# Kernel tuning notes

Measured on AMD Instinct MI355X. Metric: run time of the kernel, lower is better.

## Reference

```python
import jax, jax.numpy as jnp
import numpy as np

B, S, H = 8, 2048, 1024
NEG = -1e10


def setup_inputs() -> dict:
    key = jax.random.key(0)
    ks = jax.random.split(key, 8)
    scale = 1.0 / np.sqrt(H)
    return {
        "x": jax.random.normal(ks[0], (B, S, H), dtype=jnp.float32),
        "pad_mask": jax.random.randint(ks[1], (B, S), 0, 2, dtype=jnp.int32),
        "Wq": jax.random.uniform(ks[2], (H, H), jnp.float32, -scale, scale),
        "bq": jax.random.uniform(ks[3], (H,), jnp.float32, -scale, scale),
        "Wk": jax.random.uniform(ks[4], (H, H), jnp.float32, -scale, scale),
        "bk": jax.random.uniform(ks[5], (H,), jnp.float32, -scale, scale),
        "Wv": jax.random.uniform(ks[6], (H, H), jnp.float32, -scale, scale),
        "bv": jax.random.uniform(ks[7], (H,), jnp.float32, -scale, scale),
    }


def reference(x, pad_mask, Wq, bq, Wk, bk, Wv, bv):
    # Linear projections (torch Linear: x @ W.T + b)
    q = x @ Wq.T + bq  # [B,S,H]
    k = x @ Wk.T + bk
    v = x @ Wv.T + bv
    weight = jnp.einsum("bid,bjd->bij", q, k)  # [B,S,S]
    seq = x.shape[1]
    # causal mask (strictly upper triangular) + padding mask over key positions
    causal = jnp.triu(jnp.ones((seq, seq), dtype=jnp.float32), k=1)  # [S,S]
    pad = pad_mask.astype(jnp.float32)[:, None, :]  # [B,1,S] -> key axis
    mask = (causal[None, :, :] + pad) > 0  # [B,S,S]
    # torch code fills BEFORE scaling; replicate exactly
    weight = jnp.where(mask, NEG, weight)
    score = jax.nn.softmax(weight / jnp.sqrt(jnp.float32(weight.shape[-1] * 0 + x.shape[-1])), axis=-1)
    return jnp.einsum("bij,bjd->bid", score, v)
```

## Files before the change

### kernel.cpp

```cpp
#include <hip/hip_runtime.h>

typedef __attribute__((ext_vector_type(8))) short short8;
typedef __attribute__((ext_vector_type(4))) short short4v;
typedef __attribute__((ext_vector_type(4))) float float4v;

typedef const __attribute__((address_space(1))) unsigned int* gptr_t;
typedef __attribute__((address_space(3))) unsigned int* lptr_t;

__device__ __forceinline__ unsigned short f2bf(float f) {
  unsigned u = __float_as_uint(f);
  u += 0x7FFFu + ((u >> 16) & 1u);
  return (unsigned short)(u >> 16);
}
__device__ __forceinline__ float bf2f(unsigned short h) {
  return __uint_as_float(((unsigned)h) << 16);
}

__global__ __launch_bounds__(256) void cvt_bf16_kernel(const float* __restrict__ in,
                                                       unsigned short* __restrict__ out,
                                                       int n4) {
  int i = blockIdx.x * 256 + threadIdx.x;
  if (i >= n4) return;
  float4v v = ((const float4v*)in)[i];
  short4v o;
  o[0] = (short)f2bf(v[0]);
  o[1] = (short)f2bf(v[1]);
  o[2] = (short)f2bf(v[2]);
  o[3] = (short)f2bf(v[3]);
  ((short4v*)out)[i] = o;
}

__global__ __launch_bounds__(256) void compact_kernel(const int* __restrict__ pad,
                                                      int* __restrict__ jmap,
                                                      int* __restrict__ cntb,
                                                      float* __restrict__ mean_x) {
  int b = blockIdx.x;
  const int* prow = pad + b * 2048;
  int t = threadIdx.x;
  float4v z = {0.f, 0.f, 0.f, 0.f};
  ((float4v*)(mean_x + b * 1024))[t] = z;
  int base = t * 8;
  int ind[8], incl[8];
  int s = 0;
#pragma unroll
  for (int e = 0; e < 8; ++e) {
    ind[e] = (prow[base + e] == 0);
    s += ind[e];
    incl[e] = s;
  }
  int lane = t & 63, wv = t >> 6;
  int v = s;
#pragma unroll
  for (int off = 1; off < 64; off <<= 1) {
    int u = __shfl_up(v, off);
    if (lane >= off) v += u;
  }
  __shared__ int wsum[4];
  if (lane == 63) wsum[wv] = v;
  __syncthreads();
  int wbase = 0;
  for (int w = 0; w < wv; ++w) wbase += wsum[w];
  int excl_base = wbase + v - s;
#pragma unroll
  for (int e = 0; e < 8; ++e) {
    int cnt_i = excl_base + incl[e];
    cntb[b * 2048 + base + e] = cnt_i;
    if (ind[e]) jmap[b * 2048 + cnt_i - 1] = base + e;
  }
}

__global__ __launch_bounds__(256) void gatherX_kernel(const unsigned short* __restrict__ xb,
                                                      const int* __restrict__ jmap,
                                                      const int* __restrict__ cntb,
                                                      unsigned short* __restrict__ xc) {
  int jc = blockIdx.x, b = blockIdx.y;
  int Nc = cntb[b * 2048 + 2047];
  int W = (Nc + 127) & ~127;
  if (jc >= W) return;
  short4v* dst = (short4v*)(xc + ((size_t)(b * 2048 + jc)) * 1024);
  if (jc < Nc) {
    int j = jmap[b * 2048 + jc];
    const short4v* src = (const short4v*)(xb + ((size_t)(b * 2048 + j)) * 1024);
    dst[threadIdx.x] = src[threadIdx.x];
  } else {
    short4v z = {0, 0, 0, 0};
    dst[threadIdx.x] = z;
  }
}

__global__ __launch_bounds__(256) void meanx_kernel(const unsigned short* __restrict__ xb,
                                                    float* __restrict__ mean_x) {
  int b = blockIdx.x, hblk = blockIdx.y, iblk = blockIdx.z;
  int h = hblk * 256 + threadIdx.x;
  float s = 0.f;
  const unsigned short* base = xb + ((size_t)b * 2048 + (size_t)iblk * 256) * 1024 + h;
  for (int i = 0; i < 256; ++i) s += bf2f(base[(size_t)i * 1024]);
  atomicAdd(&mean_x[b * 1024 + h], s);
}

__global__ __launch_bounds__(256) void gemv_kernel(const float* __restrict__ mean_x,
                                                   const unsigned short* __restrict__ wv,
                                                   const float* __restrict__ bv,
                                                   float* __restrict__ fixmean) {
  int b = blockIdx.x, dblk = blockIdx.y;
  int d = dblk * 256 + threadIdx.x;
  const unsigned short* wrow = wv + (size_t)d * 1024;
  const float* mx = mean_x + b * 1024;
  float s = 0.f;
  for (int h = 0; h < 1024; h += 8) {
    short8 w = *(const short8*)(wrow + h);
#pragma unroll
    for (int e = 0; e < 8; ++e) s += mx[h + e] * bf2f(((const unsigned short*)&w)[e]);
  }
  fixmean[b * 1024 + d] = s * (1.0f / 2048.0f) + bv[d];
}

template <int MODE>
__global__ __launch_bounds__(256, 4) void gemm_bt_kernel(
    const unsigned short* __restrict__ A, const unsigned short* __restrict__ B,
    const float* __restrict__ bias1, const float* __restrict__ bias2,
    void* __restrict__ C, unsigned short* __restrict__ C2, const int* __restrict__ cnt,
    int K, int lda, int ldb, int ldc, size_t sA, size_t sB, size_t sC) {
  int bx = blockIdx.x, by = blockIdx.y, bz = blockIdx.z;
  if (MODE == 0) {
    int wg = by * 8 + bx;
    int s = (wg & 7) * 128 + (wg >> 3);
    bx = s & 7;
    by = s >> 3;
  }
  if (MODE == 1) {
    int wg = by * 16 + bx;
    int s = (wg & 7) * 32 + (wg >> 3);
    bx = s & 15;
    by = s >> 4;
  }
  int Kend = K;
  if (MODE == 1) {
    int Nc = cnt[(bz << 11) + 2047];
    if (by * 128 >= Nc) return;
  }
  if (MODE == 2) {
    int tc = cnt[(bz << 11) + (by * 128 + 127)];
    if (bx * 128 >= tc) return;
  }
  if (MODE == 3) {
    int tc = cnt[(bz << 11) + (by * 128 + 127)];
    Kend = (tc + 63) & ~63;
  }

  __shared__ __align__(16) char lds[32768];
  char* ldsA = lds;
  char* ldsB = lds + 16384;

  int tid = threadIdx.x;
  int wave = tid >> 6, lane = tid & 63;
  int lm = lane & 15, g = lane >> 4;
  int wm = wave >> 1, wn = wave & 1;
  int swl = (lm & 7) << 4;

  float4v acc[4][4];
#pragma unroll
  for (int i = 0; i < 4; ++i)
#pragma unroll
    for (int j = 0; j < 4; ++j) {
      float4v z = {0.f, 0.f, 0.f, 0.f};
      acc[i][j] = z;
    }

  const char* Abase = (const char*)(A + sA * (size_t)bz + (size_t)(by * 128) * (size_t)lda);
  const char* Bbase = (const char*)(B + sB * (size_t)bz + (size_t)(bx * 128) * (size_t)ldb);
  size_t strideA = (size_t)lda * 2u;
  size_t strideB = (size_t)ldb * 2u;

  int Lbase = wave * 1024 + lane * 16;

  for (int kt = 0; kt < Kend; kt += 64) {
#pragma unroll
    for (int c = 0; c < 4; ++c) {
      int L = c * 4096 + Lbase;
      int row = L >> 7;
      int lb = (L & 127) ^ ((row & 7) << 4);
      const char* ga = Abase + (size_t)row * strideA + (size_t)(kt * 2) + lb;
      __builtin_amdgcn_global_load_lds((gptr_t)(const void*)ga,
                                       (lptr_t)(void*)(ldsA + c * 4096 + wave * 1024), 16, 0, 0);
      const char* gb = Bbase + (size_t)row * strideB + (size_t)(kt * 2) + lb;
      __builtin_amdgcn_global_load_lds((gptr_t)(const void*)gb,
                                       (lptr_t)(void*)(ldsB + c * 4096 + wave * 1024), 16, 0, 0);
    }
    __syncthreads();

#pragma unroll
    for (int k0 = 0; k0 < 64; k0 += 32) {
      short8 af[4], bfv[4];
      int b0 = (k0 * 2 + 16 * g) ^ swl;
#pragma unroll
      for (int mi = 0; mi < 4; ++mi) {
        const char* p = ldsA + (wm * 64 + mi * 16 + lm) * 128;
        af[mi] = *(const short8*)(p + b0);
      }
#pragma unroll
      for (int ni = 0; ni < 4; ++ni) {
        const char* p = ldsB + (wn * 64 + ni * 16 + lm) * 128;
        bfv[ni] = *(const short8*)(p + b0);
      }
#pragma unroll
      for (int mi = 0; mi < 4; ++mi)
#pragma unroll
        for (int ni = 0; ni < 4; ++ni)
          acc[mi][ni] =
              __builtin_amdgcn_mfma_f32_16x16x32_bf16(af[mi], bfv[ni], acc[mi][ni], 0, 0, 0);
    }
    __syncthreads();
  }

  int mb = by * 128 + wm * 64 + g * 4;
  int nb = bx * 128 + wn * 64 + lm;
#pragma unroll
  for (int mi = 0; mi < 4; ++mi) {
#pragma unroll
    for (int ni = 0; ni < 4; ++ni) {
      int n = nb + ni * 16;
      float bias = 0.0f;
      if (MODE == 0) bias = bias1[n];
      if (MODE == 1) {
        int nn = n & 1023;
        bias = (n < 1024) ? bias1[nn] : bias2[nn];
      }
#pragma unroll
      for (int r = 0; r < 4; ++r) {
        int m = mb + mi * 16 + r;
        float v = acc[mi][ni][r] + bias;
        if (MODE == 0) {
          ((unsigned short*)C)[(size_t)m * (size_t)ldc + n] = f2bf(v);
        } else if (MODE == 1) {
          if (n < 1024) {
            ((unsigned short*)C)[sC * (size_t)bz + (size_t)m * 1024u + n] = f2bf(v);
          } else {
            size_t idx = ((size_t)bz << 21) + ((size_t)(n - 1024) << 11) + (size_t)m;
            C2[idx] = f2bf(v);
          }
        } else if (MODE == 2) {
          ((unsigned short*)C)[sC * (size_t)bz + (size_t)m * (size_t)ldc + n] = f2bf(v);
        } else {
          ((float*)C)[sC * (size_t)bz + (size_t)m * (size_t)ldc + n] = v;
        }
      }
    }
  }
}

__global__ __launch_bounds__(256) void softmax_kernel(unsigned short* __restrict__ sp,
                                                      const int* __restrict__ cntb) {
  int i = blockIdx.x, b = blockIdx.y;
  int cnt_i = cntb[b * 2048 + i];
  int tcnt = cntb[b * 2048 + (i | 127)];
  int W = (tcnt + 127) & ~127;
  unsigned short* row = sp + ((size_t)b * 2048 + (size_t)i) * 2048;
  int tid = threadIdx.x;
  int j0 = tid * 8;
  bool active = (j0 < W);

  float t[8];
  if (active) {
    short8 sv = *(const short8*)(row + j0);
#pragma unroll
    for (int e = 0; e < 8; ++e) {
      int jc = j0 + e;
      bool msk = (jc >= cnt_i);
      float raw = bf2f(((const unsigned short*)&sv)[e]);
      t[e] = (msk ? -1e10f : raw) * 0.03125f;
    }
  } else {
#pragma unroll
    for (int e = 0; e < 8; ++e) t[e] = -1e10f * 0.03125f;
  }

  float m = t[0];
#pragma unroll
  for (int e = 1; e < 8; ++e) m = fmaxf(m, t[e]);
#pragma unroll
  for (int o = 32; o > 0; o >>= 1) m = fmaxf(m, __shfl_xor(m, o));
  __shared__ float redm[4], reds[4];
  int wv = tid >> 6, ln = tid & 63;
  if (ln == 0) redm[wv] = m;
  __syncthreads();
  m = fmaxf(fmaxf(redm[0], redm[1]), fmaxf(redm[2], redm[3]));

  float p[8];
  float s = 0.f;
#pragma unroll
  for (int e = 0; e < 8; ++e) {
    p[e] = __expf(t[e] - m);
    s += p[e];
  }
#pragma unroll
  for (int o = 32; o > 0; o >>= 1) s += __shfl_xor(s, o);
  if (ln == 0) reds[wv] = s;
  __syncthreads();
  s = reds[0] + reds[1] + reds[2] + reds[3];
  float inv = 1.0f / s;

  if (active) {
    short8 ov;
#pragma unroll
    for (int e = 0; e < 8; ++e) ((unsigned short*)&ov)[e] = (short)f2bf(p[e] * inv);
    *(short8*)(row + j0) = ov;
  }
}

__global__ __launch_bounds__(256) void fixup_apply_kernel(const int* __restrict__ cntb,
                                                          const float* __restrict__ fixmean,
                                                          float* __restrict__ out) {
  int b = blockIdx.x, dchunk = blockIdx.y;
  int d = dchunk * 256 + threadIdx.x;
  float val = fixmean[b * 1024 + d];
  for (int i = 0; i < 2048; ++i) {
    if (cntb[b * 2048 + i] != 0) break;
    out[((size_t)b * 2048 + (size_t)i) * 1024 + d] = val;
  }
}

extern "C" void kernel_launch(void* const* d_in, const int* in_sizes, int n_in,
                              void* d_out, int out_size, void* d_ws, size_t ws_size,
                              hipStream_t stream) {
  const float* x = (const float*)d_in[0];
  const int* pad = (const int*)d_in[1];
  const float* Wq = (const float*)d_in[2];
  const float* bq = (const float*)d_in[3];
  const float* Wk = (const float*)d_in[4];
  const float* bk = (const float*)d_in[5];
  const float* Wv = (const float*)d_in[6];
  const float* bv = (const float*)d_in[7];
  float* out = (float*)d_out;

  char* ws = (char*)d_ws;
  unsigned short* xb  = (unsigned short*)(ws + 0);
  unsigned short* kc  = (unsigned short*)(ws + 0);
  unsigned short* xc  = (unsigned short*)(ws + 33554432);
  unsigned short* wb  = (unsigned short*)(ws + 67108864);
  int*   jmap    = (int*)(ws + 73400320);
  int*   cntb    = (int*)(ws + 73465856);
  float* mean_x  = (float*)(ws + 73531392);
  float* fixmean = (float*)(ws + 73564160);
  unsigned short* qb  = (unsigned short*)(ws + 75497472);
  unsigned short* vtc = (unsigned short*)(ws + 109051904);
  unsigned short* sp  = (unsigned short*)(ws + 142606336);

  cvt_bf16_kernel<<<16384, 256, 0, stream>>>(x, xb, 4194304);
  cvt_bf16_kernel<<<1024, 256, 0, stream>>>(Wq, wb, 262144);
  cvt_bf16_kernel<<<1024, 256, 0, stream>>>(Wk, wb + 1048576, 262144);
  cvt_bf16_kernel<<<1024, 256, 0, stream>>>(Wv, wb + 2097152, 262144);

  compact_kernel<<<8, 256, 0, stream>>>(pad, jmap, cntb, mean_x);
  dim3 gx(2048, 8);
  gatherX_kernel<<<gx, 256, 0, stream>>>(xb, jmap, cntb, xc);
  dim3 gmx(8, 4, 8);
  meanx_kernel<<<gmx, 256, 0, stream>>>(xb, mean_x);

  dim3 g1(8, 128, 1);
  gemm_bt_kernel<0><<<g1, 256, 0, stream>>>(xb, wb, bq, nullptr, qb, nullptr, nullptr,
                                            1024, 1024, 1024, 1024, 0, 0, 0);

  dim3 g2(16, 16, 8);
  gemm_bt_kernel<1><<<g2, 256, 0, stream>>>(xc, wb + 1048576, bk, bv, kc, vtc, cntb,
                                            1024, 1024, 1024, 1024, 2097152, 0, 2097152);

  dim3 g3(8, 4);
  gemv_kernel<<<g3, 256, 0, stream>>>(mean_x, wb + 2097152, bv, fixmean);

  dim3 g4(16, 16, 8);
  gemm_bt_kernel<2><<<g4, 256, 0, stream>>>(qb, kc, nullptr, nullptr, sp, nullptr, cntb,
                                            1024, 1024, 1024, 2048, 2097152, 2097152, 4194304);

  dim3 g5(2048, 8);
  softmax_kernel<<<g5, 256, 0, stream>>>(sp, cntb);

  dim3 g6(8, 16, 8);
  gemm_bt_kernel<3><<<g6, 256, 0, stream>>>(sp, vtc, nullptr, nullptr, out, nullptr, cntb,
                                            2048, 2048, 2048, 1024, 4194304, 2097152, 2097152);

  fixup_apply_kernel<<<g3, 256, 0, stream>>>(cntb, fixmean, out);
}
```

Before: 330.4 us.

## Fuse Q projection and compacted K/V projection into one GEMM launch

Merges the separate Q-projection GEMM and the compacted K/V-projection GEMM into a single launch with a 24-column grid over the concatenated Wq/Wk/Wv weights. Column tiles for K and V read from the compacted X and skip row tiles beyond the per-batch valid count. The epilogue routes output to Q, K (new buffer) or transposed V. This removes one kernel launch and lets the two GEMMs fill the GPU together, at the cost of extra branching and a new workgroup-swizzle mapping.

```diff
diff --git a/kernel.cpp b/kernel.cpp
--- a/kernel.cpp
+++ b/kernel.cpp
@@ -117,33 +117,32 @@
 
 template <int MODE>
 __global__ __launch_bounds__(256, 4) void gemm_bt_kernel(
-    const unsigned short* __restrict__ A, const unsigned short* __restrict__ B,
-    const float* __restrict__ bias1, const float* __restrict__ bias2,
-    void* __restrict__ C, unsigned short* __restrict__ C2, const int* __restrict__ cnt,
+    const unsigned short* __restrict__ A, const unsigned short* __restrict__ A2,
+    const unsigned short* __restrict__ B,
+    const float* __restrict__ b1, const float* __restrict__ b2, const float* __restrict__ b3,
+    void* __restrict__ C, unsigned short* __restrict__ C2, unsigned short* __restrict__ C3,
+    const int* __restrict__ cnt,
     int K, int lda, int ldb, int ldc, size_t sA, size_t sB, size_t sC) {
   int bx = blockIdx.x, by = blockIdx.y, bz = blockIdx.z;
+  const unsigned short* Aptr = A;
   if (MODE == 0) {
-    int wg = by * 8 + bx;
-    int s = (wg & 7) * 128 + (wg >> 3);
-    bx = s & 7;
-    by = s >> 3;
-  }
-  if (MODE == 1) {
-    int wg = by * 16 + bx;
-    int s = (wg & 7) * 32 + (wg >> 3);
-    bx = s & 15;
-    by = s >> 4;
+    int wg = by * 24 + bx;
+    int s = (wg & 7) * 384 + (wg >> 3);
+    bx = s % 24;
+    by = s / 24;
+    int r = bx >> 3;
+    if (r > 0) {
+      int b = by >> 4;
+      if (((by & 15) << 7) >= cnt[(b << 11) + 2047]) return;
+      Aptr = A2;
+    }
   }
   int Kend = K;
   if (MODE == 1) {
-    int Nc = cnt[(bz << 11) + 2047];
-    if (by * 128 >= Nc) return;
-  }
-  if (MODE == 2) {
     int tc = cnt[(bz << 11) + (by * 128 + 127)];
     if (bx * 128 >= tc) return;
   }
-  if (MODE == 3) {
+  if (MODE == 2) {
     int tc = cnt[(bz << 11) + (by * 128 + 127)];
     Kend = (tc + 63) & ~63;
   }
@@ -167,7 +166,7 @@
       acc[i][j] = z;
     }
 
-  const char* Abase = (const char*)(A + sA * (size_t)bz + (size_t)(by * 128) * (size_t)lda);
+  const char* Abase = (const char*)(Aptr + sA * (size_t)bz + (size_t)(by * 128) * (size_t)lda);
   const char* Bbase = (const char*)(B + sB * (size_t)bz + (size_t)(bx * 128) * (size_t)ldb);
   size_t strideA = (size_t)lda * 2u;
   size_t strideB = (size_t)ldb * 2u;
@@ -221,25 +220,27 @@
     for (int ni = 0; ni < 4; ++ni) {
       int n = nb + ni * 16;
       float bias = 0.0f;
-      if (MODE == 0) bias = bias1[n];
-      if (MODE == 1) {
+      if (MODE == 0) {
         int nn = n & 1023;
-        bias = (n < 1024) ? bias1[nn] : bias2[nn];
+        int r = n >> 10;
+        bias = (r == 0) ? b1[nn] : ((r == 1) ? b2[nn] : b3[nn]);
       }
 #pragma unroll
-      for (int r = 0; r < 4; ++r) {
-        int m = mb + mi * 16 + r;
-        float v = acc[mi][ni][r] + bias;
+      for (int r4 = 0; r4 < 4; ++r4) {
+        int m = mb + mi * 16 + r4;
+        float v = acc[mi][ni][r4] + bias;
         if (MODE == 0) {
-          ((unsigned short*)C)[(size_t)m * (size_t)ldc + n] = f2bf(v);
-        } else if (MODE == 1) {
-          if (n < 1024) {
-            ((unsigned short*)C)[sC * (size_t)bz + (size_t)m * 1024u + n] = f2bf(v);
+          int nn = n & 1023;
+          int r = n >> 10;
+          if (r == 0) {
+            ((unsigned short*)C)[(size_t)m * 1024u + nn] = f2bf(v);
+          } else if (r == 1) {
+            C3[(size_t)m * 1024u + nn] = f2bf(v);
           } else {
-            size_t idx = ((size_t)bz << 21) + ((size_t)(n - 1024) << 11) + (size_t)m;
+            size_t idx = ((size_t)(m >> 11) << 21) + ((size_t)nn << 11) + (size_t)(m & 2047);
             C2[idx] = f2bf(v);
           }
-        } else if (MODE == 2) {
+        } else if (MODE == 1) {
           ((unsigned short*)C)[sC * (size_t)bz + (size_t)m * (size_t)ldc + n] = f2bf(v);
         } else {
           ((float*)C)[sC * (size_t)bz + (size_t)m * (size_t)ldc + n] = v;
@@ -345,6 +346,7 @@
   unsigned short* qb  = (unsigned short*)(ws + 75497472);
   unsigned short* vtc = (unsigned short*)(ws + 109051904);
   unsigned short* sp  = (unsigned short*)(ws + 142606336);
+  unsigned short* kcb = (unsigned short*)(ws + 209715200);
 
   cvt_bf16_kernel<<<16384, 256, 0, stream>>>(x, xb, 4194304);
   cvt_bf16_kernel<<<1024, 256, 0, stream>>>(Wq, wb, 262144);
@@ -357,26 +359,24 @@
   dim3 gmx(8, 4, 8);
   meanx_kernel<<<gmx, 256, 0, stream>>>(xb, mean_x);
 
-  dim3 g1(8, 128, 1);
-  gemm_bt_kernel<0><<<g1, 256, 0, stream>>>(xb, wb, bq, nullptr, qb, nullptr, nullptr,
+  dim3 g1(24, 128, 1);
+  gemm_bt_kernel<0><<<g1, 256, 0, stream>>>(xb, xc, wb, bq, bk, bv, qb, vtc, kcb, cntb,
                                             1024, 1024, 1024, 1024, 0, 0, 0);
-
-  dim3 g2(16, 16, 8);
-  gemm_bt_kernel<1><<<g2, 256, 0, stream>>>(xc, wb + 1048576, bk, bv, kc, vtc, cntb,
-                                            1024, 1024, 1024, 1024, 2097152, 0, 2097152);
 
   dim3 g3(8, 4);
   gemv_kernel<<<g3, 256, 0, stream>>>(mean_x, wb + 2097152, bv, fixmean);
 
   dim3 g4(16, 16, 8);
-  gemm_bt_kernel<2><<<g4, 256, 0, stream>>>(qb, kc, nullptr, nullptr, sp, nullptr, cntb,
+  gemm_bt_kernel<1><<<g4, 256, 0, stream>>>(qb, nullptr, kcb, nullptr, nullptr, nullptr,
+                                            sp, nullptr, nullptr, cntb,
                                             1024, 1024, 1024, 2048, 2097152, 2097152, 4194304);
 
   dim3 g5(2048, 8);
   softmax_kernel<<<g5, 256, 0, stream>>>(sp, cntb);
 
   dim3 g6(8, 16, 8);
-  gemm_bt_kernel<3><<<g6, 256, 0, stream>>>(sp, vtc, nullptr, nullptr, out, nullptr, cntb,
+  gemm_bt_kernel<2><<<g6, 256, 0, stream>>>(sp, nullptr, vtc, nullptr, nullptr, nullptr,
+                                            out, nullptr, nullptr, cntb,
                                             2048, 2048, 2048, 1024, 4194304, 2097152, 2097152);
 
   fixup_apply_kernel<<<g3, 256, 0, stream>>>(cntb, fixmean, out);
```

Result: faster. 300.7 us (-9.0%).
